# Performance work log

Hardware: AMD Instinct MI355X
Metric: run time of the kernel (lower is better)

Reference implementation:

```python
import jax, jax.numpy as jnp
import numpy as np

B, N, D, H, FN, NL = 8, 512, 128, 64, 3, 3
OUT = 10


def setup_inputs() -> dict:
    key = jax.random.key(0)
    ks = jax.random.split(key, 20)
    X = jax.random.normal(ks[0], (B, N, D), dtype=jnp.float32)
    a = jax.random.uniform(ks[1], (B, N, N))
    A = (a < 0.02).astype(jnp.float32)
    A = jnp.maximum(A, jnp.swapaxes(A, 1, 2)) * (1.0 - jnp.eye(N, dtype=jnp.float32))
    w = lambda k, s: jax.random.normal(k, s, dtype=jnp.float32) * 0.05
    z = lambda s: jnp.zeros(s, jnp.float32)
    return {
        'X': X, 'A': A, 'p': 10,
        'curv_W1': w(ks[2], (D, H)), 'curv_b1': z((H,)),
        'curv_W2': w(ks[3], (H, 1)), 'curv_b2': z((1,)),
        'wm_W1': w(ks[4], (1, 64)), 'wm_b1': z((64,)),
        'wm_W2': w(ks[5], (64, 32)), 'wm_b2': z((32,)),
        'wm_W3': w(ks[6], (32, 1)), 'wm_b3': z((1,)),
        'fn_W1': w(ks[7], (FN, D, H)), 'fn_b1': z((FN, H)),
        'fn_W2': w(ks[8], (FN, H, 1)), 'fn_b2': z((FN, 1)),
        'gin_eps': z((NL,)),
        'gin0_W1': w(ks[9], (D, H)), 'gin0_b1': z((H,)),
        'gin0_W2': w(ks[10], (H, H)), 'gin0_b2': z((H,)),
        'gin1_W1': w(ks[11], (H, H)), 'gin1_b1': z((H,)),
        'gin1_W2': w(ks[12], (H, H)), 'gin1_b2': z((H,)),
        'gin2_W1': w(ks[13], (H, H)), 'gin2_b1': z((H,)),
        'gin2_W2': w(ks[14], (H, H)), 'gin2_b2': z((H,)),
        'out_W': w(ks[15], (D + H * NL, OUT)), 'out_b': z((OUT,)),
    }


def _curv_mlp(x, W1, b1, W2, b2):
    # MLP(nfeat->nhid->1) followed by sigmoid
    return jax.nn.sigmoid(jax.nn.relu(x @ W1 + b1) @ W2 + b2)


def _weight_mlp(A, W1, b1, W2, b2, W3, b3):
    # per-entry scalar MLP over adjacency: [B,N,N] -> [B,N,N]
    x = jax.nn.relu(A[..., None] * W1[0] + b1)  # [B,N,N,64]
    x = jax.nn.relu(x @ W2 + b2)                # [B,N,N,32]
    return jax.nn.sigmoid(x @ W3 + b3)[..., 0]


def _mv(w, v):
    return jnp.einsum('bij,bj->bi', w, v)


def _curvature_terms(f, w):
    # Algebraically identical to the torch O(N^2) expanded version, but
    # expressed with matvec contractions to avoid redundant [B,N,N] temps.
    deg = w.sum(axis=2)
    wf = _mv(w, f)
    # gamma_i = 0.5 sum_j w_ij (f_j - f_i)^2
    gamma = 0.5 * (f * f * deg - 2.0 * f * wf + _mv(w, f * f))
    # delta_f_i = sum_j w_ij (f_i - f_j)
    delta_f = f * deg - wf
    # delta_gamma_i = sum_j w_ij (gamma_i - gamma_j)
    delta_gamma = gamma * deg - _mv(w, gamma)
    # gfd_i = 0.5 sum_j w_ij (f_i - f_j)(delta_f_i - delta_f_j)
    gfd = 0.5 * (f * delta_f * deg - f * _mv(w, delta_f)
                 - delta_f * wf + _mv(w, f * delta_f))
    gamma2 = 0.5 * delta_gamma - gfd
    return gamma, gamma2


def _prune(A, kap, pct):
    num = int(N * pct / 100)  # static under jit (pct is a Python int)
    _, idx = jax.lax.top_k(kap, num)
    mask = jnp.ones((B, N), A.dtype).at[jnp.arange(B)[:, None], idx].set(0.0)
    return A * mask[:, :, None] * mask[:, None, :]


def _forward(X, A, curv_W1, curv_b1, curv_W2, curv_b2,
             wm_W1, wm_b1, wm_W2, wm_b2, wm_W3, wm_b3,
             fn_W1, fn_b1, fn_W2, fn_b2, gin_eps,
             gin0_W1, gin0_b1, gin0_W2, gin0_b2,
             gin1_W1, gin1_b1, gin1_W2, gin1_b2,
             gin2_W1, gin2_b1, gin2_W2, gin2_b2,
             out_W, out_b, p):
    kappa = _curv_mlp(X, curv_W1, curv_b1, curv_W2, curv_b2)  # [B,N,1]
    kap = kappa[..., 0]
    weights = _weight_mlp(A, wm_W1, wm_b1, wm_W2, wm_b2, wm_W3, wm_b3) * A
    curv_loss = jnp.float32(0.0)
    for i in range(FN):
        f = _curv_mlp(X, fn_W1[i], fn_b1[i], fn_W2[i], fn_b2[i])[..., 0]
        gamma, gamma2 = _curvature_terms(f, weights)
        curv_loss = curv_loss + jax.nn.relu(kap * gamma - gamma2).sum() - kappa.sum()
    gins = [(gin0_W1, gin0_b1, gin0_W2, gin0_b2),
            (gin1_W1, gin1_b1, gin1_W2, gin1_b2),
            (gin2_W1, gin2_b1, gin2_W2, gin2_b2)]
    h, A_cur, hiddens = X, A, [X]
    for t in range(NL):
        W1, b1, W2, b2 = gins[t]
        # GIN: MLP((1+eps) x + A x); dropout is identity (eval/deterministic)
        agg = (1.0 + gin_eps[t]) * h + jnp.einsum('bij,bjd->bid', A_cur, h)
        h = jax.nn.relu(jax.nn.relu(agg @ W1 + b1) @ W2 + b2)
        A_cur = _prune(A_cur, kap, p * (t + 1))
        hiddens.append(h)
    out = jnp.concatenate(hiddens, axis=2).sum(axis=1) @ out_W + out_b
    return out, curv_loss


def reference(X, A, p, curv_W1, curv_b1, curv_W2, curv_b2,
              wm_W1, wm_b1, wm_W2, wm_b2, wm_W3, wm_b3,
              fn_W1, fn_b1, fn_W2, fn_b2, gin_eps,
              gin0_W1, gin0_b1, gin0_W2, gin0_b2,
              gin1_W1, gin1_b1, gin1_W2, gin1_b2,
              gin2_W1, gin2_b1, gin2_W2, gin2_b2,
              out_W, out_b):
    return _forward(X, A, curv_W1, curv_b1, curv_W2, curv_b2,
                    wm_W1, wm_b1, wm_W2, wm_b2, wm_W3, wm_b3,
                    fn_W1, fn_b1, fn_W2, fn_b2, gin_eps,
                    gin0_W1, gin0_b1, gin0_W2, gin0_b2,
                    gin1_W1, gin1_b1, gin1_W2, gin1_b2,
                    gin2_W1, gin2_b1, gin2_W2, gin2_b2,
                    out_W, out_b, p)
```

## Files before the change

kernel.cpp:

```cpp
#include <hip/hip_runtime.h>
#include <math.h>

#define BATCH 8
#define NNODE 512
#define BN 4096
#define DIM 128
#define HID 64
#define CAP 64

__device__ __forceinline__ float sigmoidf(float x) {
  return 1.f / (1.f + expf(-x));
}
__device__ __forceinline__ float wave_sum(float v) {
  for (int off = 1; off < 64; off <<= 1) v += __shfl_xor(v, off, 64);
  return v;
}

template <int CIN, bool MASKED, int SOFF>
__device__ __forceinline__ void gin_block(
    float* smem, int node0, const float* hin, const float* W1g,
    const float* b1, const float* W2g, const float* b2, float eps1,
    const int* csr, const int* cnt, const float* mask, float* hout,
    float* Ssum) {
  float* W1s = smem;
  float* aggs = smem + CIN * HID;
  float* zs = aggs + 8 * CIN;
  int tid = threadIdx.x, wave = tid >> 6, lane = tid & 63;
  for (int t = tid; t < CIN * HID / 4; t += 256)
    ((float4*)W1s)[t] = ((const float4*)W1g)[t];
  for (int i = 0; i < 2; i++) {
    int ln = wave * 2 + i;
    int r = node0 + ln;
    int b9 = r & ~(NNODE - 1);
    const float* hi = hin + (size_t)r * CIN;
    float a0 = eps1 * hi[lane];
    float a1 = (CIN == 128) ? eps1 * hi[lane + 64] : 0.f;
    int n = cnt[r];
    const int* nb = csr + r * CAP;
    float mrow = MASKED ? mask[r] : 1.f;
    float s0 = 0.f, s1 = 0.f;
    for (int t = 0; t < n; t += 8) {
      int4 ja = *(const int4*)&nb[t];
      int4 jb = *(const int4*)&nb[t + 4];
      int r0 = b9 + ja.x, r1 = b9 + ja.y, r2 = b9 + ja.z, r3 = b9 + ja.w;
      int r4 = b9 + jb.x, r5 = b9 + jb.y, r6 = b9 + jb.z, r7 = b9 + jb.w;
      float m0 = MASKED ? mask[r0] : 1.f;
      float m1 = (t + 1 < n) ? (MASKED ? mask[r1] : 1.f) : 0.f;
      float m2 = (t + 2 < n) ? (MASKED ? mask[r2] : 1.f) : 0.f;
      float m3 = (t + 3 < n) ? (MASKED ? mask[r3] : 1.f) : 0.f;
      float m4 = (t + 4 < n) ? (MASKED ? mask[r4] : 1.f) : 0.f;
      float m5 = (t + 5 < n) ? (MASKED ? mask[r5] : 1.f) : 0.f;
      float m6 = (t + 6 < n) ? (MASKED ? mask[r6] : 1.f) : 0.f;
      float m7 = (t + 7 < n) ? (MASKED ? mask[r7] : 1.f) : 0.f;
      const float* p0 = hin + (size_t)r0 * CIN;
      const float* p1 = hin + (size_t)r1 * CIN;
      const float* p2 = hin + (size_t)r2 * CIN;
      const float* p3 = hin + (size_t)r3 * CIN;
      const float* p4 = hin + (size_t)r4 * CIN;
      const float* p5 = hin + (size_t)r5 * CIN;
      const float* p6 = hin + (size_t)r6 * CIN;
      const float* p7 = hin + (size_t)r7 * CIN;
      s0 += m0 * p0[lane] + m1 * p1[lane] + m2 * p2[lane] + m3 * p3[lane] +
            m4 * p4[lane] + m5 * p5[lane] + m6 * p6[lane] + m7 * p7[lane];
      if (CIN == 128)
        s1 += m0 * p0[lane + 64] + m1 * p1[lane + 64] + m2 * p2[lane + 64] +
              m3 * p3[lane + 64] + m4 * p4[lane + 64] + m5 * p5[lane + 64] +
              m6 * p6[lane + 64] + m7 * p7[lane + 64];
    }
    a0 += mrow * s0;
    if (CIN == 128) a1 += mrow * s1;
    aggs[ln * CIN + lane] = a0;
    if (CIN == 128) aggs[ln * CIN + 64 + lane] = a1;
  }
  __syncthreads();
  const float* x0 = aggs + (wave * 2 + 0) * CIN;
  const float* x1 = aggs + (wave * 2 + 1) * CIN;
  float bb = b1[lane];
  float acc0 = bb, acc1 = bb;
  for (int k = 0; k < CIN; k += 4) {
    float w0 = W1s[(k + 0) * HID + lane];
    float w1 = W1s[(k + 1) * HID + lane];
    float w2 = W1s[(k + 2) * HID + lane];
    float w3 = W1s[(k + 3) * HID + lane];
    float4 a;
    a = *(const float4*)&x0[k];
    acc0 += a.x * w0 + a.y * w1 + a.z * w2 + a.w * w3;
    a = *(const float4*)&x1[k];
    acc1 += a.x * w0 + a.y * w1 + a.z * w2 + a.w * w3;
  }
  zs[(wave * 2 + 0) * HID + lane] = fmaxf(0.f, acc0);
  zs[(wave * 2 + 1) * HID + lane] = fmaxf(0.f, acc1);
  const float* z0 = zs + (wave * 2 + 0) * HID;
  const float* z1 = zs + (wave * 2 + 1) * HID;
  float b2b = b2[lane];
  float c0 = b2b, c1v = b2b;
  for (int k = 0; k < HID; k += 4) {
    float w0 = W2g[(k + 0) * HID + lane];
    float w1 = W2g[(k + 1) * HID + lane];
    float w2 = W2g[(k + 2) * HID + lane];
    float w3 = W2g[(k + 3) * HID + lane];
    float4 a;
    a = *(const float4*)&z0[k];
    c0 += a.x * w0 + a.y * w1 + a.z * w2 + a.w * w3;
    a = *(const float4*)&z1[k];
    c1v += a.x * w0 + a.y * w1 + a.z * w2 + a.w * w3;
  }
  float h0 = fmaxf(0.f, c0), h1v = fmaxf(0.f, c1v);
  size_t rb = (size_t)(node0 + wave * 2) * HID + lane;
  hout[rb + 0 * HID] = h0;
  hout[rb + 1 * HID] = h1v;
  zs[(wave * 2) * HID + lane] = h0 + h1v;
  __syncthreads();
  if (tid < HID) {
    float tot = zs[0 * HID + tid] + zs[2 * HID + tid] + zs[4 * HID + tid] +
                zs[6 * HID + tid];
    atomicAdd(&Ssum[(node0 >> 9) * 320 + SOFF + tid], tot);
  }
}

__global__ __launch_bounds__(256) void k_stage1(
    const float* X, const float* A, const float* cW1, const float* cb1,
    const float* cW2, const float* cb2, const float* fW1, const float* fb1,
    const float* fW2, const float* fb2, const float* wm_W1, const float* wm_b1,
    const float* wm_W2, const float* wm_b2, const float* wm_W3,
    const float* wm_b3, float* kap, float* f, float* c1_out, int* csr,
    int* cnt_arr, float* deg, float* Ssum) {
  __shared__ float smem[10240];
  int bid = blockIdx.x;
  int tid = threadIdx.x, wave = tid >> 6, lane = tid & 63;
  if (bid < 1024) {
    int m = bid >> 8;
    int grp = bid & 255;
    float* W1s = smem;
    float* xs = smem + 8192;
    int node0 = grp * 16;
    const float* W1 = (m == 0) ? cW1 : fW1 + (size_t)(m - 1) * DIM * HID;
    for (int t = tid; t < 16 * DIM / 4; t += 256)
      ((float4*)xs)[t] = ((const float4*)(X + (size_t)node0 * DIM))[t];
    for (int t = tid; t < DIM * HID / 4; t += 256)
      ((float4*)W1s)[t] = ((const float4*)W1)[t];
    __syncthreads();
    const float* b1 = (m == 0) ? cb1 : fb1 + (m - 1) * HID;
    const float* W2 = (m == 0) ? cW2 : fW2 + (m - 1) * HID;
    float b2v = (m == 0) ? cb2[0] : fb2[m - 1];
    const float* x0 = xs + (wave * 4 + 0) * DIM;
    const float* x1 = xs + (wave * 4 + 1) * DIM;
    const float* x2 = xs + (wave * 4 + 2) * DIM;
    const float* x3 = xs + (wave * 4 + 3) * DIM;
    float w2l = W2[lane];
    float bb = b1[lane];
    float acc0 = bb, acc1 = bb, acc2 = bb, acc3 = bb;
    for (int k = 0; k < DIM; k += 4) {
      float w0 = W1s[(k + 0) * HID + lane];
      float w1 = W1s[(k + 1) * HID + lane];
      float w2 = W1s[(k + 2) * HID + lane];
      float w3 = W1s[(k + 3) * HID + lane];
      float4 a;
      a = *(const float4*)&x0[k];
      acc0 += a.x * w0 + a.y * w1 + a.z * w2 + a.w * w3;
      a = *(const float4*)&x1[k];
      acc1 += a.x * w0 + a.y * w1 + a.z * w2 + a.w * w3;
      a = *(const float4*)&x2[k];
      acc2 += a.x * w0 + a.y * w1 + a.z * w2 + a.w * w3;
      a = *(const float4*)&x3[k];
      acc3 += a.x * w0 + a.y * w1 + a.z * w2 + a.w * w3;
    }
    float s0 = wave_sum(fmaxf(0.f, acc0) * w2l);
    float s1 = wave_sum(fmaxf(0.f, acc1) * w2l);
    float s2 = wave_sum(fmaxf(0.f, acc2) * w2l);
    float s3 = wave_sum(fmaxf(0.f, acc3) * w2l);
    if (lane < 4) {
      float sv = (lane == 0) ? s0 : (lane == 1) ? s1 : (lane == 2) ? s2 : s3;
      float s = sigmoidf(sv + b2v);
      int node = node0 + wave * 4 + lane;
      if (m == 0) kap[node] = s;
      else f[node * 3 + (m - 1)] = s;
    }
    return;
  }
  if (bid < 2048) {
    int r = (bid - 1024) * 4 + wave;
    const float* row = A + (size_t)r * NNODE;
    int base = r * CAP, cnt = 0;
    for (int c = 0; c < NNODE / 64; c++) {
      int j = c * 64 + lane;
      bool nz = (row[j] != 0.f);
      unsigned long long mb = __ballot(nz);
      if (nz) {
        int pos = __popcll(mb & ((1ull << lane) - 1ull));
        int slot = cnt + pos;
        if (slot < CAP) csr[base + slot] = j;
      }
      cnt += (int)__popcll(mb);
    }
    int cc = cnt < CAP ? cnt : CAP;
    if (lane >= cc) csr[base + lane] = 0;
    if (lane == 0) {
      cnt_arr[r] = cc;
      deg[r] = (float)cnt;
    }
    return;
  }
  for (int t = tid; t < BATCH * 320; t += 256) Ssum[t] = 0.f;
  float* u = smem;
  float* y = smem + 64;
  int l = tid;
  if (l < 64) u[l] = fmaxf(0.f, wm_W1[l] + wm_b1[l]);
  __syncthreads();
  if (l < 32) {
    float a = wm_b2[l];
    for (int k = 0; k < 64; k++) a += u[k] * wm_W2[k * 32 + l];
    y[l] = fmaxf(0.f, a);
  }
  __syncthreads();
  if (l == 0) {
    float a = wm_b3[0];
    for (int k = 0; k < 32; k++) a += y[k] * wm_W3[k];
    *c1_out = sigmoidf(a);
  }
}

__global__ __launch_bounds__(256) void k_stage2(
    const float* X, const float* f, const float* kap, const int* p_ptr,
    const int* csr, const int* cnt, const float* deg, const float* c1p,
    const float* g0_W1, const float* g0_b1, const float* g0_W2,
    const float* g0_b2, const float* gin_eps, float* loss_part, float* M1,
    float* M2, float* h1, float* Ssum) {
  __shared__ float smem[9728];
  int bid = blockIdx.x;
  int tid = threadIdx.x;
  int wave = tid >> 6, lane = tid & 63;
  if (bid < BATCH) {
    int b = bid;
    float* fv = smem;
    float* ggv = smem + 1536;
    float* s1v = smem + 6144;
    float* part = smem + 7680;
    for (int t = tid; t < NNODE * 3; t += 256)
      fv[t] = f[b * NNODE * 3 + t];
    __syncthreads();
    float c1 = *c1p;
    for (int rr = 0; rr < 2; rr++) {
      int r = tid * 2 + rr;
      int gr = b * NNODE + r;
      int n = cnt[gr];
      const int* nb = csr + gr * CAP;
      float s1[3] = {0, 0, 0}, s2[3] = {0, 0, 0};
      for (int t = 0; t < n; t += 4) {
        int4 j4 = *(const int4*)&nb[t];
        float w1 = (t + 1 < n) ? 1.f : 0.f;
        float w2 = (t + 2 < n) ? 1.f : 0.f;
        float w3 = (t + 3 < n) ? 1.f : 0.f;
        const float* p0 = &fv[j4.x * 3];
        const float* p1 = &fv[j4.y * 3];
        const float* p2 = &fv[j4.z * 3];
        const float* p3 = &fv[j4.w * 3];
        for (int i = 0; i < 3; i++) {
          float v0 = p0[i], v1 = p1[i], v2 = p2[i], v3 = p3[i];
          s1[i] += v0 + w1 * v1 + w2 * v2 + w3 * v3;
          s2[i] += v0 * v0 + w1 * v1 * v1 + w2 * v2 * v2 + w3 * v3 * v3;
        }
      }
      float dA = deg[gr];
      for (int i = 0; i < 3; i++) {
        float fi = fv[r * 3 + i];
        float gamma = 0.5f * c1 * (fi * fi * dA - 2.f * fi * s1[i] + s2[i]);
        float df = c1 * (fi * dA - s1[i]);
        ggv[r * 9 + i * 3 + 0] = gamma;
        ggv[r * 9 + i * 3 + 1] = df;
        ggv[r * 9 + i * 3 + 2] = fi * df;
        s1v[r * 3 + i] = s1[i];
      }
    }
    __syncthreads();
    float local = 0.f;
    for (int rr = 0; rr < 2; rr++) {
      int r = tid * 2 + rr;
      int gr = b * NNODE + r;
      int n = cnt[gr];
      const int* nb = csr + gr * CAP;
      float T[9];
      for (int c = 0; c < 9; c++) T[c] = 0.f;
      for (int t = 0; t < n; t += 4) {
        int4 j4 = *(const int4*)&nb[t];
        float w1 = (t + 1 < n) ? 1.f : 0.f;
        float w2 = (t + 2 < n) ? 1.f : 0.f;
        float w3 = (t + 3 < n) ? 1.f : 0.f;
        const float* g0 = &ggv[j4.x * 9];
        const float* g1 = &ggv[j4.y * 9];
        const float* g2 = &ggv[j4.z * 9];
        const float* g3 = &ggv[j4.w * 9];
        for (int c = 0; c < 9; c++)
          T[c] += g0[c] + w1 * g1[c] + w2 * g2[c] + w3 * g3[c];
      }
      float dA = deg[gr];
      float kp = kap[gr];
      for (int i = 0; i < 3; i++) {
        float fi = fv[r * 3 + i];
        float s1 = s1v[r * 3 + i];
        float gamma = ggv[r * 9 + i * 3 + 0];
        float df = ggv[r * 9 + i * 3 + 1];
        float dgamma = c1 * (gamma * dA - T[i * 3 + 0]);
        float gfd = 0.5f * c1 * (fi * df * dA - fi * T[i * 3 + 1] -
                                 df * s1 + T[i * 3 + 2]);
        float gamma2 = 0.5f * dgamma - gfd;
        local += fmaxf(0.f, kp * gamma - gamma2);
      }
      local -= 3.f * kp;
    }
    local = wave_sum(local);
    if (lane == 0) part[wave] = local;
    __syncthreads();
    if (tid == 0) loss_part[b] = part[0] + part[1] + part[2] + part[3];
    return;
  }
  if (bid < 2 * BATCH) {
    int b = bid - BATCH;
    float* ks = smem;
    for (int t = tid; t < NNODE; t += 256) ks[t] = kap[b * NNODE + t];
    __syncthreads();
    int p = *p_ptr;
    int num1 = (NNODE * p) / 100;
    int num2 = (NNODE * 2 * p) / 100;
    int numm = num1 > num2 ? num1 : num2;
    for (int i = tid; i < NNODE; i += 256) {
      float v = ks[i];
      int rank = 0;
      for (int j = 0; j < NNODE; j++) {
        float u = ks[j];
        rank += (u > v) || (u == v && j < i);
      }
      M1[b * NNODE + i] = (rank < num1) ? 0.f : 1.f;
      M2[b * NNODE + i] = (rank < numm) ? 0.f : 1.f;
    }
    return;
  }
  if (bid < 2 * BATCH + 512) {
    gin_block<DIM, false, 128>(smem, (bid - 2 * BATCH) * 8, X, g0_W1, g0_b1,
                               g0_W2, g0_b2, 1.f + gin_eps[0], csr, cnt,
                               nullptr, h1, Ssum);
    return;
  }
  int idx = bid - (2 * BATCH + 512);
  int b = idx >> 3, sl = idx & 7;
  int col = tid & 127, rg = tid >> 7;
  const float* xb = X + (size_t)b * NNODE * DIM;
  int n0 = sl * 64;
  float s = 0.f;
  for (int n = n0 + rg; n < n0 + 64; n += 2) s += xb[(size_t)n * DIM + col];
  smem[tid] = s;
  __syncthreads();
  if (tid < 128)
    atomicAdd(&Ssum[b * 320 + col], smem[tid] + smem[tid + 128]);
}

__global__ __launch_bounds__(256) void k_stage3(
    const float* h1, const float* g1_W1, const float* g1_b1,
    const float* g1_W2, const float* g1_b2, const float* gin_eps,
    const int* csr, const int* cnt, const float* M1, float* h2, float* Ssum) {
  __shared__ float smem[5120];
  gin_block<HID, true, 192>(smem, blockIdx.x * 8, h1, g1_W1, g1_b1, g1_W2,
                            g1_b2, 1.f + gin_eps[1], csr, cnt, M1, h2, Ssum);
}

__global__ __launch_bounds__(256) void k_stage4(
    const float* h2, const float* g2_W1, const float* g2_b1,
    const float* g2_W2, const float* g2_b2, const float* gin_eps,
    const int* csr, const int* cnt, const float* M2, float* h3, float* Ssum) {
  __shared__ float smem[5120];
  gin_block<HID, true, 256>(smem, blockIdx.x * 8, h2, g2_W1, g2_b1, g2_W2,
                            g2_b2, 1.f + gin_eps[2], csr, cnt, M2, h3, Ssum);
}

__global__ __launch_bounds__(320) void k_out(
    const float* Ssum, const float* out_W, const float* out_b,
    const float* loss_part, float* out) {
  int b = blockIdx.x;
  int t = threadIdx.x;
  __shared__ float S[320];
  S[t] = Ssum[b * 320 + t];
  __syncthreads();
  if (t < 10) {
    float acc = out_b[t];
    for (int d = 0; d < 320; d++) acc += S[d] * out_W[d * 10 + t];
    out[b * 10 + t] = acc;
  }
  if (b == 0 && t == 0) {
    float ls = 0.f;
    for (int i = 0; i < BATCH; i++) ls += loss_part[i];
    out[80] = ls;
  }
}

extern "C" void kernel_launch(void* const* d_in, const int* in_sizes, int n_in,
                              void* d_out, int out_size, void* d_ws,
                              size_t ws_size, hipStream_t stream) {
  const float* X       = (const float*)d_in[0];
  const float* A       = (const float*)d_in[1];
  const int*   p       = (const int*)d_in[2];
  const float* curv_W1 = (const float*)d_in[3];
  const float* curv_b1 = (const float*)d_in[4];
  const float* curv_W2 = (const float*)d_in[5];
  const float* curv_b2 = (const float*)d_in[6];
  const float* wm_W1   = (const float*)d_in[7];
  const float* wm_b1   = (const float*)d_in[8];
  const float* wm_W2   = (const float*)d_in[9];
  const float* wm_b2   = (const float*)d_in[10];
  const float* wm_W3   = (const float*)d_in[11];
  const float* wm_b3   = (const float*)d_in[12];
  const float* fn_W1   = (const float*)d_in[13];
  const float* fn_b1   = (const float*)d_in[14];
  const float* fn_W2   = (const float*)d_in[15];
  const float* fn_b2   = (const float*)d_in[16];
  const float* gin_eps = (const float*)d_in[17];
  const float* g0_W1   = (const float*)d_in[18];
  const float* g0_b1   = (const float*)d_in[19];
  const float* g0_W2   = (const float*)d_in[20];
  const float* g0_b2   = (const float*)d_in[21];
  const float* g1_W1   = (const float*)d_in[22];
  const float* g1_b1   = (const float*)d_in[23];
  const float* g1_W2   = (const float*)d_in[24];
  const float* g1_b2   = (const float*)d_in[25];
  const float* g2_W1   = (const float*)d_in[26];
  const float* g2_b1   = (const float*)d_in[27];
  const float* g2_W2   = (const float*)d_in[28];
  const float* g2_b2   = (const float*)d_in[29];
  const float* out_W   = (const float*)d_in[30];
  const float* out_b   = (const float*)d_in[31];
  float* out = (float*)d_out;

  float* ws = (float*)d_ws;
  size_t o = 0;
  float* loss_part = ws + o; o += 16;
  float* c1       = ws + o; o += 16;
  float* Ssum     = ws + o; o += BATCH * 320 + 16;
  float* kap      = ws + o; o += BN;
  float* f        = ws + o; o += (size_t)BN * 3 + 16;
  float* deg      = ws + o; o += BN;
  float* M1       = ws + o; o += BN;
  float* M2       = ws + o; o += BN;
  float* h1       = ws + o; o += (size_t)BN * HID;
  float* h2       = ws + o; o += (size_t)BN * HID;
  float* h3       = ws + o; o += (size_t)BN * HID;
  int* cnt  = (int*)(ws + o); o += BN;
  int* csr  = (int*)(ws + o); o += (size_t)BN * CAP;

  k_stage1<<<2049, 256, 0, stream>>>(
      X, A, curv_W1, curv_b1, curv_W2, curv_b2, fn_W1, fn_b1, fn_W2, fn_b2,
      wm_W1, wm_b1, wm_W2, wm_b2, wm_W3, wm_b3, kap, f, c1, csr, cnt, deg,
      Ssum);
  k_stage2<<<2 * BATCH + 512 + 64, 256, 0, stream>>>(
      X, f, kap, p, csr, cnt, deg, c1, g0_W1, g0_b1, g0_W2, g0_b2, gin_eps,
      loss_part, M1, M2, h1, Ssum);
  k_stage3<<<512, 256, 0, stream>>>(h1, g1_W1, g1_b1, g1_W2, g1_b2, gin_eps,
                                    csr, cnt, M1, h2, Ssum);
  k_stage4<<<512, 256, 0, stream>>>(h2, g2_W1, g2_b1, g2_W2, g2_b2, gin_eps,
                                    csr, cnt, M2, h3, Ssum);
  k_out<<<BATCH, 320, 0, stream>>>(Ssum, out_W, out_b, loss_part, out);
}
```

Measured before the change: 195.4 us.

## Fuse all stages into one persistent cooperative kernel with grid syncs

Replaces the five back-to-back kernel launches with a single cooperative kernel of 512 blocks. Each block loops over the former per-stage block indices, and the stages are separated by grid-wide barriers. This removes launch gaps and inter-kernel drain and fill time. The tradeoff is that each stage now runs on only 512 persistent blocks at capped occupancy, and grid sync has its own cost. A fallback to the multi-kernel path runs if the cooperative launch fails.

```diff
diff --git a/kernel.cpp b/kernel.cpp
--- a/kernel.cpp
+++ b/kernel.cpp
@@ -1,5 +1,8 @@
 #include <hip/hip_runtime.h>
+#include <hip/hip_cooperative_groups.h>
 #include <math.h>
+
+namespace cg = cooperative_groups;
 
 #define BATCH 8
 #define NNODE 512
@@ -15,6 +18,22 @@
   for (int off = 1; off < 64; off <<= 1) v += __shfl_xor(v, off, 64);
   return v;
 }
+
+struct Prm {
+  const float *X, *A;
+  const int *p;
+  const float *cW1, *cb1, *cW2, *cb2;
+  const float *wm_W1, *wm_b1, *wm_W2, *wm_b2, *wm_W3, *wm_b3;
+  const float *fW1, *fb1, *fW2, *fb2;
+  const float *gin_eps;
+  const float *g0_W1, *g0_b1, *g0_W2, *g0_b2;
+  const float *g1_W1, *g1_b1, *g1_W2, *g1_b2;
+  const float *g2_W1, *g2_b1, *g2_W2, *g2_b2;
+  const float *out_W, *out_b;
+  float *out;
+  float *loss_part, *c1, *Ssum, *kap, *f, *deg, *M1, *M2, *h1, *h2, *h3;
+  int *cnt, *csr;
+};
 
 template <int CIN, bool MASKED, int SOFF>
 __device__ __forceinline__ void gin_block(
@@ -118,343 +137,375 @@
   }
 }
 
-__global__ __launch_bounds__(256) void k_stage1(
-    const float* X, const float* A, const float* cW1, const float* cb1,
-    const float* cW2, const float* cb2, const float* fW1, const float* fb1,
-    const float* fW2, const float* fb2, const float* wm_W1, const float* wm_b1,
-    const float* wm_W2, const float* wm_b2, const float* wm_W3,
-    const float* wm_b3, float* kap, float* f, float* c1_out, int* csr,
-    int* cnt_arr, float* deg, float* Ssum) {
-  __shared__ float smem[10240];
-  int bid = blockIdx.x;
+__device__ __forceinline__ void mlp_task(int m, int grp, const Prm& p,
+                                         float* smem) {
   int tid = threadIdx.x, wave = tid >> 6, lane = tid & 63;
-  if (bid < 1024) {
-    int m = bid >> 8;
-    int grp = bid & 255;
-    float* W1s = smem;
-    float* xs = smem + 8192;
-    int node0 = grp * 16;
-    const float* W1 = (m == 0) ? cW1 : fW1 + (size_t)(m - 1) * DIM * HID;
-    for (int t = tid; t < 16 * DIM / 4; t += 256)
-      ((float4*)xs)[t] = ((const float4*)(X + (size_t)node0 * DIM))[t];
-    for (int t = tid; t < DIM * HID / 4; t += 256)
-      ((float4*)W1s)[t] = ((const float4*)W1)[t];
-    __syncthreads();
-    const float* b1 = (m == 0) ? cb1 : fb1 + (m - 1) * HID;
-    const float* W2 = (m == 0) ? cW2 : fW2 + (m - 1) * HID;
-    float b2v = (m == 0) ? cb2[0] : fb2[m - 1];
-    const float* x0 = xs + (wave * 4 + 0) * DIM;
-    const float* x1 = xs + (wave * 4 + 1) * DIM;
-    const float* x2 = xs + (wave * 4 + 2) * DIM;
-    const float* x3 = xs + (wave * 4 + 3) * DIM;
-    float w2l = W2[lane];
-    float bb = b1[lane];
-    float acc0 = bb, acc1 = bb, acc2 = bb, acc3 = bb;
-    for (int k = 0; k < DIM; k += 4) {
-      float w0 = W1s[(k + 0) * HID + lane];
-      float w1 = W1s[(k + 1) * HID + lane];
-      float w2 = W1s[(k + 2) * HID + lane];
-      float w3 = W1s[(k + 3) * HID + lane];
-      float4 a;
-      a = *(const float4*)&x0[k];
-      acc0 += a.x * w0 + a.y * w1 + a.z * w2 + a.w * w3;
-      a = *(const float4*)&x1[k];
-      acc1 += a.x * w0 + a.y * w1 + a.z * w2 + a.w * w3;
-      a = *(const float4*)&x2[k];
-      acc2 += a.x * w0 + a.y * w1 + a.z * w2 + a.w * w3;
-      a = *(const float4*)&x3[k];
-      acc3 += a.x * w0 + a.y * w1 + a.z * w2 + a.w * w3;
-    }
-    float s0 = wave_sum(fmaxf(0.f, acc0) * w2l);
-    float s1 = wave_sum(fmaxf(0.f, acc1) * w2l);
-    float s2 = wave_sum(fmaxf(0.f, acc2) * w2l);
-    float s3 = wave_sum(fmaxf(0.f, acc3) * w2l);
-    if (lane < 4) {
-      float sv = (lane == 0) ? s0 : (lane == 1) ? s1 : (lane == 2) ? s2 : s3;
-      float s = sigmoidf(sv + b2v);
-      int node = node0 + wave * 4 + lane;
-      if (m == 0) kap[node] = s;
-      else f[node * 3 + (m - 1)] = s;
-    }
-    return;
-  }
-  if (bid < 2048) {
-    int r = (bid - 1024) * 4 + wave;
-    const float* row = A + (size_t)r * NNODE;
-    int base = r * CAP, cnt = 0;
-    for (int c = 0; c < NNODE / 64; c++) {
-      int j = c * 64 + lane;
-      bool nz = (row[j] != 0.f);
-      unsigned long long mb = __ballot(nz);
-      if (nz) {
-        int pos = __popcll(mb & ((1ull << lane) - 1ull));
-        int slot = cnt + pos;
-        if (slot < CAP) csr[base + slot] = j;
-      }
-      cnt += (int)__popcll(mb);
-    }
-    int cc = cnt < CAP ? cnt : CAP;
-    if (lane >= cc) csr[base + lane] = 0;
-    if (lane == 0) {
-      cnt_arr[r] = cc;
-      deg[r] = (float)cnt;
-    }
-    return;
-  }
-  for (int t = tid; t < BATCH * 320; t += 256) Ssum[t] = 0.f;
+  float* W1s = smem;
+  float* xs = smem + 8192;
+  int node0 = grp * 16;
+  const float* W1 = (m == 0) ? p.cW1 : p.fW1 + (size_t)(m - 1) * DIM * HID;
+  for (int t = tid; t < 16 * DIM / 4; t += 256)
+    ((float4*)xs)[t] = ((const float4*)(p.X + (size_t)node0 * DIM))[t];
+  for (int t = tid; t < DIM * HID / 4; t += 256)
+    ((float4*)W1s)[t] = ((const float4*)W1)[t];
+  __syncthreads();
+  const float* b1 = (m == 0) ? p.cb1 : p.fb1 + (m - 1) * HID;
+  const float* W2 = (m == 0) ? p.cW2 : p.fW2 + (m - 1) * HID;
+  float b2v = (m == 0) ? p.cb2[0] : p.fb2[m - 1];
+  const float* x0 = xs + (wave * 4 + 0) * DIM;
+  const float* x1 = xs + (wave * 4 + 1) * DIM;
+  const float* x2 = xs + (wave * 4 + 2) * DIM;
+  const float* x3 = xs + (wave * 4 + 3) * DIM;
+  float w2l = W2[lane];
+  float bb = b1[lane];
+  float acc0 = bb, acc1 = bb, acc2 = bb, acc3 = bb;
+  for (int k = 0; k < DIM; k += 4) {
+    float w0 = W1s[(k + 0) * HID + lane];
+    float w1 = W1s[(k + 1) * HID + lane];
+    float w2 = W1s[(k + 2) * HID + lane];
+    float w3 = W1s[(k + 3) * HID + lane];
+    float4 a;
+    a = *(const float4*)&x0[k];
+    acc0 += a.x * w0 + a.y * w1 + a.z * w2 + a.w * w3;
+    a = *(const float4*)&x1[k];
+    acc1 += a.x * w0 + a.y * w1 + a.z * w2 + a.w * w3;
+    a = *(const float4*)&x2[k];
+    acc2 += a.x * w0 + a.y * w1 + a.z * w2 + a.w * w3;
+    a = *(const float4*)&x3[k];
+    acc3 += a.x * w0 + a.y * w1 + a.z * w2 + a.w * w3;
+  }
+  float s0 = wave_sum(fmaxf(0.f, acc0) * w2l);
+  float s1 = wave_sum(fmaxf(0.f, acc1) * w2l);
+  float s2 = wave_sum(fmaxf(0.f, acc2) * w2l);
+  float s3 = wave_sum(fmaxf(0.f, acc3) * w2l);
+  if (lane < 4) {
+    float sv = (lane == 0) ? s0 : (lane == 1) ? s1 : (lane == 2) ? s2 : s3;
+    float s = sigmoidf(sv + b2v);
+    int node = node0 + wave * 4 + lane;
+    if (m == 0) p.kap[node] = s;
+    else p.f[node * 3 + (m - 1)] = s;
+  }
+}
+
+__device__ __forceinline__ void csr_task(int idx, const Prm& p) {
+  int tid = threadIdx.x, wave = tid >> 6, lane = tid & 63;
+  int r = idx * 4 + wave;
+  const float* row = p.A + (size_t)r * NNODE;
+  int base = r * CAP, cnt = 0;
+  for (int c = 0; c < NNODE / 64; c++) {
+    int j = c * 64 + lane;
+    bool nz = (row[j] != 0.f);
+    unsigned long long mb = __ballot(nz);
+    if (nz) {
+      int pos = __popcll(mb & ((1ull << lane) - 1ull));
+      int slot = cnt + pos;
+      if (slot < CAP) p.csr[base + slot] = j;
+    }
+    cnt += (int)__popcll(mb);
+  }
+  int cc = cnt < CAP ? cnt : CAP;
+  if (lane >= cc) p.csr[base + lane] = 0;
+  if (lane == 0) {
+    p.cnt[r] = cc;
+    p.deg[r] = (float)cnt;
+  }
+}
+
+__device__ __forceinline__ void c1_zero_task(const Prm& p, float* smem) {
+  int tid = threadIdx.x;
+  for (int t = tid; t < BATCH * 320; t += 256) p.Ssum[t] = 0.f;
   float* u = smem;
   float* y = smem + 64;
   int l = tid;
-  if (l < 64) u[l] = fmaxf(0.f, wm_W1[l] + wm_b1[l]);
+  if (l < 64) u[l] = fmaxf(0.f, p.wm_W1[l] + p.wm_b1[l]);
   __syncthreads();
   if (l < 32) {
-    float a = wm_b2[l];
-    for (int k = 0; k < 64; k++) a += u[k] * wm_W2[k * 32 + l];
+    float a = p.wm_b2[l];
+    for (int k = 0; k < 64; k++) a += u[k] * p.wm_W2[k * 32 + l];
     y[l] = fmaxf(0.f, a);
   }
   __syncthreads();
   if (l == 0) {
-    float a = wm_b3[0];
-    for (int k = 0; k < 32; k++) a += y[k] * wm_W3[k];
-    *c1_out = sigmoidf(a);
-  }
-}
-
-__global__ __launch_bounds__(256) void k_stage2(
-    const float* X, const float* f, const float* kap, const int* p_ptr,
-    const int* csr, const int* cnt, const float* deg, const float* c1p,
-    const float* g0_W1, const float* g0_b1, const float* g0_W2,
-    const float* g0_b2, const float* gin_eps, float* loss_part, float* M1,
-    float* M2, float* h1, float* Ssum) {
-  __shared__ float smem[9728];
-  int bid = blockIdx.x;
+    float a = p.wm_b3[0];
+    for (int k = 0; k < 32; k++) a += y[k] * p.wm_W3[k];
+    *p.c1 = sigmoidf(a);
+  }
+}
+
+__device__ __forceinline__ void curv_task(int b, const Prm& p, float* smem) {
+  int tid = threadIdx.x, wave = tid >> 6, lane = tid & 63;
+  float* fv = smem;
+  float* ggv = smem + 1536;
+  float* s1v = smem + 6144;
+  float* part = smem + 7680;
+  for (int t = tid; t < NNODE * 3; t += 256)
+    fv[t] = p.f[b * NNODE * 3 + t];
+  __syncthreads();
+  float c1 = *p.c1;
+  for (int rr = 0; rr < 2; rr++) {
+    int r = tid * 2 + rr;
+    int gr = b * NNODE + r;
+    int n = p.cnt[gr];
+    const int* nb = p.csr + gr * CAP;
+    float s1[3] = {0, 0, 0}, s2[3] = {0, 0, 0};
+    for (int t = 0; t < n; t += 4) {
+      int4 j4 = *(const int4*)&nb[t];
+      float w1 = (t + 1 < n) ? 1.f : 0.f;
+      float w2 = (t + 2 < n) ? 1.f : 0.f;
+      float w3 = (t + 3 < n) ? 1.f : 0.f;
+      const float* p0 = &fv[j4.x * 3];
+      const float* p1 = &fv[j4.y * 3];
+      const float* p2 = &fv[j4.z * 3];
+      const float* p3 = &fv[j4.w * 3];
+      for (int i = 0; i < 3; i++) {
+        float v0 = p0[i], v1 = p1[i], v2 = p2[i], v3 = p3[i];
+        s1[i] += v0 + w1 * v1 + w2 * v2 + w3 * v3;
+        s2[i] += v0 * v0 + w1 * v1 * v1 + w2 * v2 * v2 + w3 * v3 * v3;
+      }
+    }
+    float dA = p.deg[gr];
+    for (int i = 0; i < 3; i++) {
+      float fi = fv[r * 3 + i];
+      float gamma = 0.5f * c1 * (fi * fi * dA - 2.f * fi * s1[i] + s2[i]);
+      float df = c1 * (fi * dA - s1[i]);
+      ggv[r * 9 + i * 3 + 0] = gamma;
+      ggv[r * 9 + i * 3 + 1] = df;
+      ggv[r * 9 + i * 3 + 2] = fi * df;
+      s1v[r * 3 + i] = s1[i];
+    }
+  }
+  __syncthreads();
+  float local = 0.f;
+  for (int rr = 0; rr < 2; rr++) {
+    int r = tid * 2 + rr;
+    int gr = b * NNODE + r;
+    int n = p.cnt[gr];
+    const int* nb = p.csr + gr * CAP;
+    float T[9];
+    for (int c = 0; c < 9; c++) T[c] = 0.f;
+    for (int t = 0; t < n; t += 4) {
+      int4 j4 = *(const int4*)&nb[t];
+      float w1 = (t + 1 < n) ? 1.f : 0.f;
+      float w2 = (t + 2 < n) ? 1.f : 0.f;
+      float w3 = (t + 3 < n) ? 1.f : 0.f;
+      const float* g0 = &ggv[j4.x * 9];
+      const float* g1 = &ggv[j4.y * 9];
+      const float* g2 = &ggv[j4.z * 9];
+      const float* g3 = &ggv[j4.w * 9];
+      for (int c = 0; c < 9; c++)
+        T[c] += g0[c] + w1 * g1[c] + w2 * g2[c] + w3 * g3[c];
+    }
+    float dA = p.deg[gr];
+    float kp = p.kap[gr];
+    for (int i = 0; i < 3; i++) {
+      float fi = fv[r * 3 + i];
+      float s1 = s1v[r * 3 + i];
+      float gamma = ggv[r * 9 + i * 3 + 0];
+      float df = ggv[r * 9 + i * 3 + 1];
+      float dgamma = c1 * (gamma * dA - T[i * 3 + 0]);
+      float gfd = 0.5f * c1 * (fi * df * dA - fi * T[i * 3 + 1] -
+                               df * s1 + T[i * 3 + 2]);
+      float gamma2 = 0.5f * dgamma - gfd;
+      local += fmaxf(0.f, kp * gamma - gamma2);
+    }
+    local -= 3.f * kp;
+  }
+  local = wave_sum(local);
+  if (lane == 0) part[wave] = local;
+  __syncthreads();
+  if (tid == 0) p.loss_part[b] = part[0] + part[1] + part[2] + part[3];
+}
+
+__device__ __forceinline__ void topk_task(int b, const Prm& p, float* smem) {
   int tid = threadIdx.x;
-  int wave = tid >> 6, lane = tid & 63;
-  if (bid < BATCH) {
-    int b = bid;
-    float* fv = smem;
-    float* ggv = smem + 1536;
-    float* s1v = smem + 6144;
-    float* part = smem + 7680;
-    for (int t = tid; t < NNODE * 3; t += 256)
-      fv[t] = f[b * NNODE * 3 + t];
-    __syncthreads();
-    float c1 = *c1p;
-    for (int rr = 0; rr < 2; rr++) {
-      int r = tid * 2 + rr;
-      int gr = b * NNODE + r;
-      int n = cnt[gr];
-      const int* nb = csr + gr * CAP;
-      float s1[3] = {0, 0, 0}, s2[3] = {0, 0, 0};
-      for (int t = 0; t < n; t += 4) {
-        int4 j4 = *(const int4*)&nb[t];
-        float w1 = (t + 1 < n) ? 1.f : 0.f;
-        float w2 = (t + 2 < n) ? 1.f : 0.f;
-        float w3 = (t + 3 < n) ? 1.f : 0.f;
-        const float* p0 = &fv[j4.x * 3];
-        const float* p1 = &fv[j4.y * 3];
-        const float* p2 = &fv[j4.z * 3];
-        const float* p3 = &fv[j4.w * 3];
-        for (int i = 0; i < 3; i++) {
-          float v0 = p0[i], v1 = p1[i], v2 = p2[i], v3 = p3[i];
-          s1[i] += v0 + w1 * v1 + w2 * v2 + w3 * v3;
-          s2[i] += v0 * v0 + w1 * v1 * v1 + w2 * v2 * v2 + w3 * v3 * v3;
-        }
-      }
-      float dA = deg[gr];
-      for (int i = 0; i < 3; i++) {
-        float fi = fv[r * 3 + i];
-        float gamma = 0.5f * c1 * (fi * fi * dA - 2.f * fi * s1[i] + s2[i]);
-        float df = c1 * (fi * dA - s1[i]);
-        ggv[r * 9 + i * 3 + 0] = gamma;
-        ggv[r * 9 + i * 3 + 1] = df;
-        ggv[r * 9 + i * 3 + 2] = fi * df;
-        s1v[r * 3 + i] = s1[i];
-      }
-    }
-    __syncthreads();
-    float local = 0.f;
-    for (int rr = 0; rr < 2; rr++) {
-      int r = tid * 2 + rr;
-      int gr = b * NNODE + r;
-      int n = cnt[gr];
-      const int* nb = csr + gr * CAP;
-      float T[9];
-      for (int c = 0; c < 9; c++) T[c] = 0.f;
-      for (int t = 0; t < n; t += 4) {
-        int4 j4 = *(const int4*)&nb[t];
-        float w1 = (t + 1 < n) ? 1.f : 0.f;
-        float w2 = (t + 2 < n) ? 1.f : 0.f;
-        float w3 = (t + 3 < n) ? 1.f : 0.f;
-        const float* g0 = &ggv[j4.x * 9];
-        const float* g1 = &ggv[j4.y * 9];
-        const float* g2 = &ggv[j4.z * 9];
-        const float* g3 = &ggv[j4.w * 9];
-        for (int c = 0; c < 9; c++)
-          T[c] += g0[c] + w1 * g1[c] + w2 * g2[c] + w3 * g3[c];
-      }
-      float dA = deg[gr];
-      float kp = kap[gr];
-      for (int i = 0; i < 3; i++) {
-        float fi = fv[r * 3 + i];
-        float s1 = s1v[r * 3 + i];
-        float gamma = ggv[r * 9 + i * 3 + 0];
-        float df = ggv[r * 9 + i * 3 + 1];
-        float dgamma = c1 * (gamma * dA - T[i * 3 + 0]);
-        float gfd = 0.5f * c1 * (fi * df * dA - fi * T[i * 3 + 1] -
-                                 df * s1 + T[i * 3 + 2]);
-        float gamma2 = 0.5f * dgamma - gfd;
-        local += fmaxf(0.f, kp * gamma - gamma2);
-      }
-      local -= 3.f * kp;
-    }
-    local = wave_sum(local);
-    if (lane == 0) part[wave] = local;
-    __syncthreads();
-    if (tid == 0) loss_part[b] = part[0] + part[1] + part[2] + part[3];
-    return;
-  }
-  if (bid < 2 * BATCH) {
-    int b = bid - BATCH;
-    float* ks = smem;
-    for (int t = tid; t < NNODE; t += 256) ks[t] = kap[b * NNODE + t];
-    __syncthreads();
-    int p = *p_ptr;
-    int num1 = (NNODE * p) / 100;
-    int num2 = (NNODE * 2 * p) / 100;
-    int numm = num1 > num2 ? num1 : num2;
-    for (int i = tid; i < NNODE; i += 256) {
-      float v = ks[i];
-      int rank = 0;
-      for (int j = 0; j < NNODE; j++) {
-        float u = ks[j];
-        rank += (u > v) || (u == v && j < i);
-      }
-      M1[b * NNODE + i] = (rank < num1) ? 0.f : 1.f;
-      M2[b * NNODE + i] = (rank < numm) ? 0.f : 1.f;
-    }
-    return;
-  }
-  if (bid < 2 * BATCH + 512) {
-    gin_block<DIM, false, 128>(smem, (bid - 2 * BATCH) * 8, X, g0_W1, g0_b1,
-                               g0_W2, g0_b2, 1.f + gin_eps[0], csr, cnt,
-                               nullptr, h1, Ssum);
-    return;
-  }
-  int idx = bid - (2 * BATCH + 512);
+  float* ks = smem;
+  for (int t = tid; t < NNODE; t += 256) ks[t] = p.kap[b * NNODE + t];
+  __syncthreads();
+  int pp = *p.p;
+  int num1 = (NNODE * pp) / 100;
+  int num2 = (NNODE * 2 * pp) / 100;
+  int numm = num1 > num2 ? num1 : num2;
+  for (int i = tid; i < NNODE; i += 256) {
+    float v = ks[i];
+    int rank = 0;
+    for (int j = 0; j < NNODE; j++) {
+      float u = ks[j];
+      rank += (u > v) || (u == v && j < i);
+    }
+    p.M1[b * NNODE + i] = (rank < num1) ? 0.f : 1.f;
+    p.M2[b * NNODE + i] = (rank < numm) ? 0.f : 1.f;
+  }
+}
+
+__device__ __forceinline__ void colsum_task(int idx, const Prm& p,
+                                            float* smem) {
+  int tid = threadIdx.x;
   int b = idx >> 3, sl = idx & 7;
   int col = tid & 127, rg = tid >> 7;
-  const float* xb = X + (size_t)b * NNODE * DIM;
+  const float* xb = p.X + (size_t)b * NNODE * DIM;
   int n0 = sl * 64;
   float s = 0.f;
   for (int n = n0 + rg; n < n0 + 64; n += 2) s += xb[(size_t)n * DIM + col];
   smem[tid] = s;
   __syncthreads();
   if (tid < 128)
-    atomicAdd(&Ssum[b * 320 + col], smem[tid] + smem[tid + 128]);
-}
-
-__global__ __launch_bounds__(256) void k_stage3(
-    const float* h1, const float* g1_W1, const float* g1_b1,
-    const float* g1_W2, const float* g1_b2, const float* gin_eps,
-    const int* csr, const int* cnt, const float* M1, float* h2, float* Ssum) {
-  __shared__ float smem[5120];
-  gin_block<HID, true, 192>(smem, blockIdx.x * 8, h1, g1_W1, g1_b1, g1_W2,
-                            g1_b2, 1.f + gin_eps[1], csr, cnt, M1, h2, Ssum);
-}
-
-__global__ __launch_bounds__(256) void k_stage4(
-    const float* h2, const float* g2_W1, const float* g2_b1,
-    const float* g2_W2, const float* g2_b2, const float* gin_eps,
-    const int* csr, const int* cnt, const float* M2, float* h3, float* Ssum) {
-  __shared__ float smem[5120];
-  gin_block<HID, true, 256>(smem, blockIdx.x * 8, h2, g2_W1, g2_b1, g2_W2,
-                            g2_b2, 1.f + gin_eps[2], csr, cnt, M2, h3, Ssum);
-}
-
-__global__ __launch_bounds__(320) void k_out(
-    const float* Ssum, const float* out_W, const float* out_b,
-    const float* loss_part, float* out) {
-  int b = blockIdx.x;
+    atomicAdd(&p.Ssum[b * 320 + col], smem[tid] + smem[tid + 128]);
+}
+
+__device__ __forceinline__ void readout_task(int b, const Prm& p,
+                                             float* smem) {
   int t = threadIdx.x;
-  __shared__ float S[320];
-  S[t] = Ssum[b * 320 + t];
+  for (int i = t; i < 320; i += 256) smem[i] = p.Ssum[b * 320 + i];
   __syncthreads();
   if (t < 10) {
-    float acc = out_b[t];
-    for (int d = 0; d < 320; d++) acc += S[d] * out_W[d * 10 + t];
-    out[b * 10 + t] = acc;
+    float acc = p.out_b[t];
+    for (int d = 0; d < 320; d++) acc += smem[d] * p.out_W[d * 10 + t];
+    p.out[b * 10 + t] = acc;
   }
   if (b == 0 && t == 0) {
     float ls = 0.f;
-    for (int i = 0; i < BATCH; i++) ls += loss_part[i];
-    out[80] = ls;
-  }
+    for (int i = 0; i < BATCH; i++) ls += p.loss_part[i];
+    p.out[80] = ls;
+  }
+}
+
+__global__ __launch_bounds__(256, 2) void k_fused(Prm p) {
+  __shared__ float smem[10240];
+  int bid = blockIdx.x, nb = gridDim.x;
+  for (int t = bid; t < 2049; t += nb) {
+    __syncthreads();
+    if (t < 1024) mlp_task(t >> 8, t & 255, p, smem);
+    else if (t < 2048) csr_task(t - 1024, p);
+    else c1_zero_task(p, smem);
+  }
+  cg::this_grid().sync();
+  for (int t = bid; t < 2 * BATCH + 512 + 64; t += nb) {
+    __syncthreads();
+    if (t < BATCH) curv_task(t, p, smem);
+    else if (t < 2 * BATCH) topk_task(t - BATCH, p, smem);
+    else if (t < 2 * BATCH + 512)
+      gin_block<DIM, false, 128>(smem, (t - 2 * BATCH) * 8, p.X, p.g0_W1,
+                                 p.g0_b1, p.g0_W2, p.g0_b2,
+                                 1.f + p.gin_eps[0], p.csr, p.cnt, nullptr,
+                                 p.h1, p.Ssum);
+    else colsum_task(t - (2 * BATCH + 512), p, smem);
+  }
+  cg::this_grid().sync();
+  for (int t = bid; t < 512; t += nb) {
+    __syncthreads();
+    gin_block<HID, true, 192>(smem, t * 8, p.h1, p.g1_W1, p.g1_b1, p.g1_W2,
+                              p.g1_b2, 1.f + p.gin_eps[1], p.csr, p.cnt,
+                              p.M1, p.h2, p.Ssum);
+  }
+  cg::this_grid().sync();
+  for (int t = bid; t < 512; t += nb) {
+    __syncthreads();
+    gin_block<HID, true, 256>(smem, t * 8, p.h2, p.g2_W1, p.g2_b1, p.g2_W2,
+                              p.g2_b2, 1.f + p.gin_eps[2], p.csr, p.cnt,
+                              p.M2, p.h3, p.Ssum);
+  }
+  cg::this_grid().sync();
+  if (bid < BATCH) readout_task(bid, p, smem);
+}
+
+__global__ __launch_bounds__(256) void k_stage1(Prm p) {
+  __shared__ float smem[10240];
+  int bid = blockIdx.x;
+  if (bid < 1024) mlp_task(bid >> 8, bid & 255, p, smem);
+  else if (bid < 2048) csr_task(bid - 1024, p);
+  else c1_zero_task(p, smem);
+}
+__global__ __launch_bounds__(256) void k_stage2(Prm p) {
+  __shared__ float smem[10240];
+  int bid = blockIdx.x;
+  if (bid < BATCH) curv_task(bid, p, smem);
+  else if (bid < 2 * BATCH) topk_task(bid - BATCH, p, smem);
+  else if (bid < 2 * BATCH + 512)
+    gin_block<DIM, false, 128>(smem, (bid - 2 * BATCH) * 8, p.X, p.g0_W1,
+                               p.g0_b1, p.g0_W2, p.g0_b2, 1.f + p.gin_eps[0],
+                               p.csr, p.cnt, nullptr, p.h1, p.Ssum);
+  else colsum_task(bid - (2 * BATCH + 512), p, smem);
+}
+__global__ __launch_bounds__(256) void k_stage3(Prm p) {
+  __shared__ float smem[10240];
+  gin_block<HID, true, 192>(smem, blockIdx.x * 8, p.h1, p.g1_W1, p.g1_b1,
+                            p.g1_W2, p.g1_b2, 1.f + p.gin_eps[1], p.csr,
+                            p.cnt, p.M1, p.h2, p.Ssum);
+}
+__global__ __launch_bounds__(256) void k_stage4(Prm p) {
+  __shared__ float smem[10240];
+  gin_block<HID, true, 256>(smem, blockIdx.x * 8, p.h2, p.g2_W1, p.g2_b1,
+                            p.g2_W2, p.g2_b2, 1.f + p.gin_eps[2], p.csr,
+                            p.cnt, p.M2, p.h3, p.Ssum);
+}
+__global__ __launch_bounds__(256) void k_out(Prm p) {
+  __shared__ float smem[10240];
+  readout_task(blockIdx.x, p, smem);
 }
 
 extern "C" void kernel_launch(void* const* d_in, const int* in_sizes, int n_in,
                               void* d_out, int out_size, void* d_ws,
                               size_t ws_size, hipStream_t stream) {
-  const float* X       = (const float*)d_in[0];
-  const float* A       = (const float*)d_in[1];
-  const int*   p       = (const int*)d_in[2];
-  const float* curv_W1 = (const float*)d_in[3];
-  const float* curv_b1 = (const float*)d_in[4];
-  const float* curv_W2 = (const float*)d_in[5];
-  const float* curv_b2 = (const float*)d_in[6];
-  const float* wm_W1   = (const float*)d_in[7];
-  const float* wm_b1   = (const float*)d_in[8];
-  const float* wm_W2   = (const float*)d_in[9];
-  const float* wm_b2   = (const float*)d_in[10];
-  const float* wm_W3   = (const float*)d_in[11];
-  const float* wm_b3   = (const float*)d_in[12];
-  const float* fn_W1   = (const float*)d_in[13];
-  const float* fn_b1   = (const float*)d_in[14];
-  const float* fn_W2   = (const float*)d_in[15];
-  const float* fn_b2   = (const float*)d_in[16];
-  const float* gin_eps = (const float*)d_in[17];
-  const float* g0_W1   = (const float*)d_in[18];
-  const float* g0_b1   = (const float*)d_in[19];
-  const float* g0_W2   = (const float*)d_in[20];
-  const float* g0_b2   = (const float*)d_in[21];
-  const float* g1_W1   = (const float*)d_in[22];
-  const float* g1_b1   = (const float*)d_in[23];
-  const float* g1_W2   = (const float*)d_in[24];
-  const float* g1_b2   = (const float*)d_in[25];
-  const float* g2_W1   = (const float*)d_in[26];
-  const float* g2_b1   = (const float*)d_in[27];
-  const float* g2_W2   = (const float*)d_in[28];
-  const float* g2_b2   = (const float*)d_in[29];
-  const float* out_W   = (const float*)d_in[30];
-  const float* out_b   = (const float*)d_in[31];
-  float* out = (float*)d_out;
+  Prm q;
+  q.X       = (const float*)d_in[0];
+  q.A       = (const float*)d_in[1];
+  q.p       = (const int*)d_in[2];
+  q.cW1     = (const float*)d_in[3];
+  q.cb1     = (const float*)d_in[4];
+  q.cW2     = (const float*)d_in[5];
+  q.cb2     = (const float*)d_in[6];
+  q.wm_W1   = (const float*)d_in[7];
+  q.wm_b1   = (const float*)d_in[8];
+  q.wm_W2   = (const float*)d_in[9];
+  q.wm_b2   = (const float*)d_in[10];
+  q.wm_W3   = (const float*)d_in[11];
+  q.wm_b3   = (const float*)d_in[12];
+  q.fW1     = (const float*)d_in[13];
+  q.fb1     = (const float*)d_in[14];
+  q.fW2     = (const float*)d_in[15];
+  q.fb2     = (const float*)d_in[16];
+  q.gin_eps = (const float*)d_in[17];
+  q.g0_W1   = (const float*)d_in[18];
+  q.g0_b1   = (const float*)d_in[19];
+  q.g0_W2   = (const float*)d_in[20];
+  q.g0_b2   = (const float*)d_in[21];
+  q.g1_W1   = (const float*)d_in[22];
+  q.g1_b1   = (const float*)d_in[23];
+  q.g1_W2   = (const float*)d_in[24];
+  q.g1_b2   = (const float*)d_in[25];
+  q.g2_W1   = (const float*)d_in[26];
+  q.g2_b1   = (const float*)d_in[27];
+  q.g2_W2   = (const float*)d_in[28];
+  q.g2_b2   = (const float*)d_in[29];
+  q.out_W   = (const float*)d_in[30];
+  q.out_b   = (const float*)d_in[31];
+  q.out     = (float*)d_out;
 
   float* ws = (float*)d_ws;
   size_t o = 0;
-  float* loss_part = ws + o; o += 16;
-  float* c1       = ws + o; o += 16;
-  float* Ssum     = ws + o; o += BATCH * 320 + 16;
-  float* kap      = ws + o; o += BN;
-  float* f        = ws + o; o += (size_t)BN * 3 + 16;
-  float* deg      = ws + o; o += BN;
-  float* M1       = ws + o; o += BN;
-  float* M2       = ws + o; o += BN;
-  float* h1       = ws + o; o += (size_t)BN * HID;
-  float* h2       = ws + o; o += (size_t)BN * HID;
-  float* h3       = ws + o; o += (size_t)BN * HID;
-  int* cnt  = (int*)(ws + o); o += BN;
-  int* csr  = (int*)(ws + o); o += (size_t)BN * CAP;
-
-  k_stage1<<<2049, 256, 0, stream>>>(
-      X, A, curv_W1, curv_b1, curv_W2, curv_b2, fn_W1, fn_b1, fn_W2, fn_b2,
-      wm_W1, wm_b1, wm_W2, wm_b2, wm_W3, wm_b3, kap, f, c1, csr, cnt, deg,
-      Ssum);
-  k_stage2<<<2 * BATCH + 512 + 64, 256, 0, stream>>>(
-      X, f, kap, p, csr, cnt, deg, c1, g0_W1, g0_b1, g0_W2, g0_b2, gin_eps,
-      loss_part, M1, M2, h1, Ssum);
-  k_stage3<<<512, 256, 0, stream>>>(h1, g1_W1, g1_b1, g1_W2, g1_b2, gin_eps,
-                                    csr, cnt, M1, h2, Ssum);
-  k_stage4<<<512, 256, 0, stream>>>(h2, g2_W1, g2_b1, g2_W2, g2_b2, gin_eps,
-                                    csr, cnt, M2, h3, Ssum);
-  k_out<<<BATCH, 320, 0, stream>>>(Ssum, out_W, out_b, loss_part, out);
-}
+  q.loss_part = ws + o; o += 16;
+  q.c1        = ws + o; o += 16;
+  q.Ssum      = ws + o; o += BATCH * 320 + 16;
+  q.kap       = ws + o; o += BN;
+  q.f         = ws + o; o += (size_t)BN * 3 + 16;
+  q.deg       = ws + o; o += BN;
+  q.M1        = ws + o; o += BN;
+  q.M2        = ws + o; o += BN;
+  q.h1        = ws + o; o += (size_t)BN * HID;
+  q.h2        = ws + o; o += (size_t)BN * HID;
+  q.h3        = ws + o; o += (size_t)BN * HID;
+  q.cnt = (int*)(ws + o); o += BN;
+  q.csr = (int*)(ws + o); o += (size_t)BN * CAP;
+
+  void* kargs[] = { (void*)&q };
+  hipError_t e = hipLaunchCooperativeKernel((const void*)k_fused, dim3(512),
+                                            dim3(256), kargs, 0, stream);
+  if (e != hipSuccess) {
+    (void)hipGetLastError();
+    k_stage1<<<2049, 256, 0, stream>>>(q);
+    k_stage2<<<2 * BATCH + 512 + 64, 256, 0, stream>>>(q);
+    k_stage3<<<512, 256, 0, stream>>>(q);
+    k_stage4<<<512, 256, 0, stream>>>(q);
+    k_out<<<BATCH, 256, 0, stream>>>(q);
+  }
+}
```

After: 462.7 us. +136.8%, slower.
